# Performance work log

Measured on AMD Instinct MI355X. Metric: run time of the kernel, lower is better.

The kernel has to match this reference:

```python
import jax, jax.numpy as jnp
import numpy as np

THRESHOLD = 0.5
NEGPOS_RATIO = 3
VARIANCES = (0.1, 0.2)

B, P, C, T = 64, 24564, 81, 50


def point_form(boxes):
    # center form (cx,cy,w,h) -> corner form (x1,y1,x2,y2)
    return jnp.concatenate([boxes[:, :2] - boxes[:, 2:] / 2,
                            boxes[:, :2] + boxes[:, 2:] / 2], axis=-1)


def jaccard(box_a, box_b):
    # box_a [T,4], box_b [P,4], corner form -> IoU [T,P]
    max_xy = jnp.minimum(box_a[:, None, 2:], box_b[None, :, 2:])
    min_xy = jnp.maximum(box_a[:, None, :2], box_b[None, :, :2])
    inter = jnp.prod(jnp.clip(max_xy - min_xy, 0.0), axis=-1)
    area_a = jnp.prod(box_a[:, 2:] - box_a[:, :2], axis=-1)[:, None]
    area_b = jnp.prod(box_b[:, 2:] - box_b[:, :2], axis=-1)[None, :]
    return inter / (area_a + area_b - inter)


def encode(matched, priors, variances):
    # matched [P,4] corner form, priors [P,4] center form
    g_cxcy = (matched[:, :2] + matched[:, 2:]) / 2 - priors[:, :2]
    g_cxcy = g_cxcy / (variances[0] * priors[:, 2:])
    g_wh = (matched[:, 2:] - matched[:, :2]) / priors[:, 2:]
    g_wh = jnp.log(g_wh) / variances[1]
    return jnp.concatenate([g_cxcy, g_wh], axis=-1)


def match_one(truths, labels, priors):
    # truths [T,4] corner, labels [T] int, priors [P,4] center form
    overlaps = jaccard(truths, point_form(priors))          # [T,P]
    best_prior_idx = jnp.argmax(overlaps, axis=1)           # [T] best prior per gt
    best_truth_overlap = jnp.max(overlaps, axis=0)          # [P]
    best_truth_idx = jnp.argmax(overlaps, axis=0)           # [P]
    # ensure every gt keeps its best prior
    best_truth_overlap = best_truth_overlap.at[best_prior_idx].set(2.0)
    best_truth_idx = best_truth_idx.at[best_prior_idx].set(jnp.arange(truths.shape[0]))
    matched = truths[best_truth_idx]                        # [P,4]
    conf = labels[best_truth_idx] + 1                       # background = 0
    conf = jnp.where(best_truth_overlap < THRESHOLD, 0, conf)
    loc = encode(matched, priors, VARIANCES)                # [P,4]
    return loc, conf


def setup_inputs() -> dict:
    key = jax.random.key(0)
    k1, k2, k3, k4, k5, k6, k7 = jax.random.split(key, 7)
    loc_data = jax.random.normal(k1, (B, P, 4), jnp.float32)
    conf_data = jax.random.normal(k2, (B, P, C), jnp.float32)
    # priors: center form, in-bounds
    ctr = 0.05 + 0.9 * jax.random.uniform(k3, (P, 2))
    wh = 0.05 + 0.25 * jax.random.uniform(k4, (P, 2))
    priors = jnp.concatenate([ctr, wh], axis=-1).astype(jnp.float32)
    # gt boxes: corner form with x2>x1, y2>y1
    xy1 = 0.7 * jax.random.uniform(k5, (B, T, 2))
    gwh = 0.05 + 0.25 * jax.random.uniform(k6, (B, T, 2))
    targets_boxes = jnp.concatenate([xy1, jnp.minimum(xy1 + gwh, 1.0)], axis=-1).astype(jnp.float32)
    targets_labels = jax.random.randint(k7, (B, T), 0, C - 1, jnp.int32)
    return {"loc_data": loc_data, "conf_data": conf_data, "priors": priors,
            "targets_boxes": targets_boxes, "targets_labels": targets_labels}


def reference(loc_data, conf_data, priors, targets_boxes, targets_labels):
    num, num_priors, _ = loc_data.shape
    # per-image matching, batched with vmap
    loc_t, conf_t = jax.vmap(lambda t, l: match_one(t, l, priors))(targets_boxes, targets_labels)
    pos = conf_t > 0                                         # [B,P]
    # localization: smooth-L1 over positives, sum
    diff = loc_data - loc_t
    ad = jnp.abs(diff)
    sl1 = jnp.where(ad < 1.0, 0.5 * diff * diff, ad - 0.5)
    loss_l = jnp.sum(sl1 * pos[..., None])
    # confidence: cross entropy = logsumexp - gathered logit
    logsm = jax.nn.log_softmax(conf_data, axis=-1)
    ce = -jnp.take_along_axis(logsm, conf_t[..., None], axis=-1)[..., 0]  # [B,P]
    # hard negative mining: rank losses among negatives
    loss_mine = jnp.where(pos, 0.0, ce)
    num_pos = jnp.sum(pos, axis=1)                           # [B]
    num_neg = jnp.minimum(NEGPOS_RATIO * num_pos, num_priors - 1)
    idx_rank = jnp.argsort(jnp.argsort(-loss_mine, axis=1), axis=1)
    neg = idx_rank < num_neg[:, None]
    loss_c = jnp.sum(jnp.where(pos | neg, ce, 0.0))
    n = jnp.maximum(jnp.sum(num_pos), 1).astype(loc_data.dtype)
    return jnp.stack([loss_l / n, loss_c / n])
```

## Files before the change

### kernel.cpp

```cpp
#include <hip/hip_runtime.h>
#include <cstdint>
#include <cstddef>

#define NB 64
#define NP 24564
#define NC 81
#define NROWS (NB*NP)
#define NT 50
#define TCH 10
#define NSEG 16
#define SEGLEN 1536
#define RPB 128

__device__ __forceinline__ unsigned long long umax64(unsigned long long a, unsigned long long b){
  return a > b ? a : b;
}

__global__ __launch_bounds__(256) void k_bestprior(
    const float* __restrict__ priors, const float* __restrict__ tboxes,
    unsigned long long* __restrict__ bpk)
{
  __shared__ float tb[TCH*4];
  __shared__ float ta[TCH];
  __shared__ unsigned long long part[4][TCH];
  const int tid = threadIdx.x;
  const int b  = blockIdx.x;
  const int t0 = blockIdx.y * TCH;
  const int i0 = blockIdx.z * SEGLEN;
  const int iend = min(i0 + SEGLEN, NP);
  if (tid < TCH*4) tb[tid] = tboxes[(b*NT + t0)*4 + tid];
  __syncthreads();
  if (tid < TCH) ta[tid] = (tb[tid*4+2]-tb[tid*4+0]) * (tb[tid*4+3]-tb[tid*4+1]);
  __syncthreads();

  unsigned long long best[TCH];
  #pragma unroll
  for (int j = 0; j < TCH; ++j) best[j] = 0ULL;

  for (int i = i0 + tid; i < iend; i += 256){
    const float4 pr = ((const float4* __restrict__)priors)[i];
    const float px1 = pr.x - 0.5f*pr.z, py1 = pr.y - 0.5f*pr.w;
    const float px2 = pr.x + 0.5f*pr.z, py2 = pr.y + 0.5f*pr.w;
    const float pa  = pr.z * pr.w;
    const unsigned long long low = (unsigned long long)(~(unsigned)i);
    #pragma unroll
    for (int j = 0; j < TCH; ++j){
      float ix = fminf(tb[j*4+2], px2) - fmaxf(tb[j*4+0], px1);
      float iy = fminf(tb[j*4+3], py2) - fmaxf(tb[j*4+1], py1);
      ix = fmaxf(ix, 0.0f); iy = fmaxf(iy, 0.0f);
      const float inter = ix * iy;
      const float iou = inter / (ta[j] + pa - inter);
      const unsigned long long key =
          ((unsigned long long)__float_as_uint(iou) << 32) | low;
      best[j] = umax64(best[j], key);
    }
  }
  #pragma unroll
  for (int off = 32; off > 0; off >>= 1){
    #pragma unroll
    for (int j = 0; j < TCH; ++j)
      best[j] = umax64(best[j], __shfl_down(best[j], off));
  }
  const int wv = tid >> 6;
  if ((tid & 63) == 0){
    #pragma unroll
    for (int j = 0; j < TCH; ++j) part[wv][j] = best[j];
  }
  __syncthreads();
  if (tid < TCH){
    const unsigned long long m =
        umax64(umax64(part[0][tid], part[1][tid]),
               umax64(part[2][tid], part[3][tid]));
    atomicMax(&bpk[b*NT + t0 + tid], m);
  }
}

__global__ __launch_bounds__(256) void k_ce(
    const float* __restrict__ conf, const float* __restrict__ loc,
    const float* __restrict__ priors, const float* __restrict__ tboxes,
    const int* __restrict__ tlabels,
    const unsigned long long* __restrict__ bpk,
    float* __restrict__ mine, float* __restrict__ ce_pos,
    float* __restrict__ loss_l, int* __restrict__ num_pos)
{
  __shared__ float4 cbuf4[(RPB*NC)/4];
  __shared__ float tb[NT*4];
  __shared__ float ta[NT];
  __shared__ int ips[NT];
  __shared__ int tl[NT];
  float* cbuf = (float*)cbuf4;

  const int tid = threadIdx.x;
  const int b  = blockIdx.y;
  const int p0 = blockIdx.x * RPB;
  const int rows = min(RPB, NP - p0);

  if (tid < NT*4) tb[tid] = tboxes[b*NT*4 + tid];
  else if (tid < NT*4 + NT){
    const int t = tid - NT*4;
    ips[t] = (int)(~(unsigned)(bpk[b*NT + t] & 0xffffffffULL));
  }

  const float4* __restrict__ csrc =
      (const float4* __restrict__)(conf + (size_t)(b*NP + p0) * NC);
  const int nf4 = (rows * NC) >> 2;
  for (int i = tid; i < nf4; i += 256) cbuf4[i] = csrc[i];
  __syncthreads();
  if (tid < NT){
    ta[tid] = (tb[tid*4+2]-tb[tid*4+0]) * (tb[tid*4+3]-tb[tid*4+1]);
    tl[tid] = tlabels[b*NT + tid];
  }
  __syncthreads();

  const int row = tid >> 1;
  const int h   = tid & 1;
  const bool active = row < rows;
  const int p = p0 + (active ? row : 0);
  const int r = b*NP + p;

  const float4 pr = ((const float4* __restrict__)priors)[p];
  const float px1 = pr.x - 0.5f*pr.z, py1 = pr.y - 0.5f*pr.w;
  const float px2 = pr.x + 0.5f*pr.z, py2 = pr.y + 0.5f*pr.w;
  const float pa  = pr.z * pr.w;
  float ov = -1.0f; int ti = 0;
  for (int t = 0; t < NT; ++t){
    float ix = fminf(tb[t*4+2], px2) - fmaxf(tb[t*4+0], px1);
    float iy = fminf(tb[t*4+3], py2) - fmaxf(tb[t*4+1], py1);
    ix = fmaxf(ix, 0.0f); iy = fmaxf(iy, 0.0f);
    const float inter = ix * iy;
    const float iou = inter / (ta[t] + pa - inter);
    if (iou > ov){ ov = iou; ti = t; }
  }
  #pragma unroll 10
  for (int t = 0; t < NT; ++t){
    if (ips[t] == p){ ov = 2.0f; ti = t; }
  }
  const int cls = (ov < 0.5f) ? 0 : (tl[ti] + 1);

  const float* __restrict__ myrow = cbuf + row * NC;
  const int c0 = 41 * h;
  float v[41];
  #pragma unroll
  for (int c = 0; c < 40; ++c) v[c] = myrow[c0 + c];
  v[40] = h ? -INFINITY : myrow[40];

  float mh = v[0];
  #pragma unroll
  for (int c = 1; c < 41; ++c) mh = fmaxf(mh, v[c]);
  const float m = fmaxf(mh, __shfl_xor(mh, 1));

  float sh = 0.0f;
  #pragma unroll
  for (int c = 0; c < 41; ++c) sh += __expf(v[c] - m);
  const float S = sh + __shfl_xor(sh, 1);

  const float lg = myrow[cls];
  const float ce = m + __logf(S) - lg;

  const bool own = active && (h == 0);
  const bool pos = own && (cls > 0);
  if (own) mine[r] = pos ? 0.0f : ce;

  float cp = pos ? ce : 0.0f;
  float ll = 0.0f;
  int   pc = pos ? 1 : 0;
  if (pos){
    const float tx1 = tb[ti*4+0], ty1 = tb[ti*4+1], tx2 = tb[ti*4+2], ty2 = tb[ti*4+3];
    const float gcx = ((tx1 + tx2)*0.5f - pr.x) / (0.1f*pr.z);
    const float gcy = ((ty1 + ty2)*0.5f - pr.y) / (0.1f*pr.w);
    const float gw  = __logf((tx2 - tx1) / pr.z) * 5.0f;
    const float gh  = __logf((ty2 - ty1) / pr.w) * 5.0f;
    const float4 ld = ((const float4* __restrict__)loc)[r];
    float d, ad;
    d = ld.x - gcx; ad = fabsf(d); ll += (ad < 1.0f) ? 0.5f*d*d : ad - 0.5f;
    d = ld.y - gcy; ad = fabsf(d); ll += (ad < 1.0f) ? 0.5f*d*d : ad - 0.5f;
    d = ld.z - gw;  ad = fabsf(d); ll += (ad < 1.0f) ? 0.5f*d*d : ad - 0.5f;
    d = ld.w - gh;  ad = fabsf(d); ll += (ad < 1.0f) ? 0.5f*d*d : ad - 0.5f;
  }

  #pragma unroll
  for (int off = 32; off > 0; off >>= 1){
    cp += __shfl_down(cp, off);
    ll += __shfl_down(ll, off);
    pc += __shfl_down(pc, off);
  }
  __shared__ float rcp[4], rll[4];
  __shared__ int rpc[4];
  const int wv = tid >> 6;
  if ((tid & 63) == 0){ rcp[wv] = cp; rll[wv] = ll; rpc[wv] = pc; }
  __syncthreads();
  if (tid == 0){
    atomicAdd(&ce_pos[b], (rcp[0]+rcp[1])+(rcp[2]+rcp[3]));
    atomicAdd(&loss_l[b], (rll[0]+rll[1])+(rll[2]+rll[3]));
    atomicAdd(&num_pos[b], (rpc[0]+rpc[1])+(rpc[2]+rpc[3]));
  }
}

__global__ __launch_bounds__(1024) void k_topk(
    const float* __restrict__ mine, const int* __restrict__ num_pos,
    float* __restrict__ topk)
{
  const int b = blockIdx.x;
  const int tid = threadIdx.x;
  const float4* __restrict__ d4 =
      (const float4* __restrict__)(mine + (size_t)b * NP);
  const int k = min(3 * num_pos[b], NP - 1);

  __shared__ unsigned hist[256];
  __shared__ unsigned s_prefix;
  __shared__ int s_rem;
  __shared__ float wsum[16];

  if (k <= 0){
    if (tid == 0) topk[b] = 0.0f;
    return;
  }
  if (tid == 0){ s_prefix = 0u; s_rem = k; }

  for (int pass = 0; pass < 4; ++pass){
    const int shift = 24 - pass*8;
    if (tid < 256) hist[tid] = 0u;
    __syncthreads();
    const unsigned pref = s_prefix;
    const int rem = s_rem;
    for (int i = tid; i < 6141; i += 1024){
      const float4 v = d4[i];
      unsigned u;
      u = __float_as_uint(v.x);
      if (pass == 0 || (u >> (shift+8)) == pref) atomicAdd(&hist[(u>>shift)&255u], 1u);
      u = __float_as_uint(v.y);
      if (pass == 0 || (u >> (shift+8)) == pref) atomicAdd(&hist[(u>>shift)&255u], 1u);
      u = __float_as_uint(v.z);
      if (pass == 0 || (u >> (shift+8)) == pref) atomicAdd(&hist[(u>>shift)&255u], 1u);
      u = __float_as_uint(v.w);
      if (pass == 0 || (u >> (shift+8)) == pref) atomicAdd(&hist[(u>>shift)&255u], 1u);
    }
    __syncthreads();
    if (tid < 64){
      const unsigned h0 = hist[4*tid], h1 = hist[4*tid+1];
      const unsigned h2 = hist[4*tid+2], h3 = hist[4*tid+3];
      const unsigned pl = h0 + h1 + h2 + h3;
      unsigned S = pl;
      #pragma unroll
      for (int off = 1; off < 64; off <<= 1){
        const unsigned v = __shfl_down(S, off);
        if (tid + off < 64) S += v;
      }
      const unsigned Sn = S - pl;
      const unsigned t3 = h3 + Sn;
      const unsigned t2 = h2 + t3;
      const unsigned t1 = h1 + t2;
      const unsigned t0 = h0 + t1;
      if ((int)t0 >= rem && (int)t1 < rem){ s_prefix = (pref<<8) | (4u*tid+0u); s_rem = rem - (int)t1; }
      if ((int)t1 >= rem && (int)t2 < rem){ s_prefix = (pref<<8) | (4u*tid+1u); s_rem = rem - (int)t2; }
      if ((int)t2 >= rem && (int)t3 < rem){ s_prefix = (pref<<8) | (4u*tid+2u); s_rem = rem - (int)t3; }
      if ((int)t3 >= rem && (int)Sn < rem){ s_prefix = (pref<<8) | (4u*tid+3u); s_rem = rem - (int)Sn; }
    }
    __syncthreads();
  }

  const unsigned kb = s_prefix;
  const int rem = s_rem;
  const float kv = __uint_as_float(kb);
  float acc = 0.0f;
  for (int i = tid; i < 6141; i += 1024){
    const float4 v = d4[i];
    if (__float_as_uint(v.x) > kb) acc += v.x;
    if (__float_as_uint(v.y) > kb) acc += v.y;
    if (__float_as_uint(v.z) > kb) acc += v.z;
    if (__float_as_uint(v.w) > kb) acc += v.w;
  }
  #pragma unroll
  for (int off = 32; off > 0; off >>= 1) acc += __shfl_down(acc, off);
  if ((tid & 63) == 0) wsum[tid >> 6] = acc;
  __syncthreads();
  if (tid == 0){
    float s = 0.0f;
    #pragma unroll
    for (int j = 0; j < 16; ++j) s += wsum[j];
    topk[b] = s + (float)rem * kv;
  }
}

__global__ void k_final(const int* __restrict__ num_pos,
                        const float* __restrict__ loss_l,
                        const float* __restrict__ ce_pos,
                        const float* __restrict__ topk,
                        float* __restrict__ out)
{
  const int tid = threadIdx.x;
  int   np = num_pos[tid];
  float ll = loss_l[tid];
  float cp = ce_pos[tid];
  float tk = topk[tid];
  #pragma unroll
  for (int off = 32; off > 0; off >>= 1){
    np += __shfl_down(np, off);
    ll += __shfl_down(ll, off);
    cp += __shfl_down(cp, off);
    tk += __shfl_down(tk, off);
  }
  if (tid == 0){
    const float n = (float)max(np, 1);
    out[0] = ll / n;
    out[1] = (cp + tk) / n;
  }
}

extern "C" void kernel_launch(void* const* d_in, const int* in_sizes, int n_in,
                              void* d_out, int out_size, void* d_ws, size_t ws_size,
                              hipStream_t stream)
{
  const float* loc     = (const float*)d_in[0];
  const float* conf    = (const float*)d_in[1];
  const float* priors  = (const float*)d_in[2];
  const float* tboxes  = (const float*)d_in[3];
  const int*   tlabels = (const int*)d_in[4];
  float* out = (float*)d_out;

  char* ws = (char*)d_ws;
  int*   num_pos = (int*)(ws + 0);
  float* loss_l  = (float*)(ws + 256);
  float* ce_pos  = (float*)(ws + 512);
  float* topk    = (float*)(ws + 768);
  unsigned long long* bpk = (unsigned long long*)(ws + 1024);
  float* mine = (float*)(ws + 26624);

  hipMemsetAsync(ws, 0, 26624, stream);

  dim3 gA(NB, NT/TCH, NSEG);
  k_bestprior<<<gA, 256, 0, stream>>>(priors, tboxes, bpk);

  dim3 gC((NP + RPB - 1)/RPB, NB);
  k_ce<<<gC, 256, 0, stream>>>(conf, loc, priors, tboxes, tlabels,
                               bpk, mine, ce_pos, loss_l, num_pos);

  k_topk<<<NB, 1024, 0, stream>>>(mine, num_pos, topk);

  k_final<<<1, 64, 0, stream>>>(num_pos, loss_l, ce_pos, topk, out);
}
```

Measured before the change: 896.6 us.

## Halve rows per block, split each row across four lanes, prefetch conf into registers

The CE kernel now handles 64 rows per block with four lanes per row, each covering about 20 classes, so fewer registers are live per thread and shared memory per block is halved, which should let more blocks run per CU. The conf tile is loaded into registers first, then the target-box setup runs, then the registers are written to LDS, and one __syncthreads is removed. Target boxes are stored as float4. The cost is twice as many blocks, so per-block setup (IoU over 50 targets, each computed redundantly by all four lanes of a row) is repeated more often, plus an extra shuffle stage in the softmax reductions.

```diff
diff --git a/kernel.cpp b/kernel.cpp
--- a/kernel.cpp
+++ b/kernel.cpp
@@ -10,7 +10,7 @@
 #define TCH 10
 #define NSEG 16
 #define SEGLEN 1536
-#define RPB 128
+#define RPB 64
 
 __device__ __forceinline__ unsigned long long umax64(unsigned long long a, unsigned long long b){
   return a > b ? a : b;
@@ -83,8 +83,8 @@
     float* __restrict__ mine, float* __restrict__ ce_pos,
     float* __restrict__ loss_l, int* __restrict__ num_pos)
 {
-  __shared__ float4 cbuf4[(RPB*NC)/4];
-  __shared__ float tb[NT*4];
+  __shared__ float4 cbuf4[(RPB*NC)/4 + 1];
+  __shared__ float4 tb4[NT];
   __shared__ float ta[NT];
   __shared__ int ips[NT];
   __shared__ int tl[NT];
@@ -95,25 +95,35 @@
   const int p0 = blockIdx.x * RPB;
   const int rows = min(RPB, NP - p0);
 
-  if (tid < NT*4) tb[tid] = tboxes[b*NT*4 + tid];
-  else if (tid < NT*4 + NT){
-    const int t = tid - NT*4;
-    ips[t] = (int)(~(unsigned)(bpk[b*NT + t] & 0xffffffffULL));
-  }
-
   const float4* __restrict__ csrc =
       (const float4* __restrict__)(conf + (size_t)(b*NP + p0) * NC);
   const int nf4 = (rows * NC) >> 2;
-  for (int i = tid; i < nf4; i += 256) cbuf4[i] = csrc[i];
-  __syncthreads();
-  if (tid < NT){
-    ta[tid] = (tb[tid*4+2]-tb[tid*4+0]) * (tb[tid*4+3]-tb[tid*4+1]);
-    tl[tid] = tlabels[b*NT + tid];
-  }
-  __syncthreads();
-
-  const int row = tid >> 1;
-  const int h   = tid & 1;
+  float4 st[6];
+  #pragma unroll
+  for (int j = 0; j < 6; ++j){
+    const int i = tid + j*256;
+    if (i < nf4) st[j] = csrc[i];
+  }
+
+  if (tid < NT*4){
+    ((float*)tb4)[tid] = tboxes[b*NT*4 + tid];
+  } else if (tid < NT*4 + NT){
+    const int t = tid - NT*4;
+    const float4 T = ((const float4* __restrict__)tboxes)[b*NT + t];
+    ta[t] = (T.z - T.x) * (T.w - T.y);
+    tl[t] = tlabels[b*NT + t];
+    ips[t] = (int)(~(unsigned)(bpk[b*NT + t] & 0xffffffffULL));
+  }
+
+  #pragma unroll
+  for (int j = 0; j < 6; ++j){
+    const int i = tid + j*256;
+    if (i < nf4) cbuf4[i] = st[j];
+  }
+  __syncthreads();
+
+  const int row = tid >> 2;
+  const int q   = tid & 3;
   const bool active = row < rows;
   const int p = p0 + (active ? row : 0);
   const int r = b*NP + p;
@@ -124,8 +134,9 @@
   const float pa  = pr.z * pr.w;
   float ov = -1.0f; int ti = 0;
   for (int t = 0; t < NT; ++t){
-    float ix = fminf(tb[t*4+2], px2) - fmaxf(tb[t*4+0], px1);
-    float iy = fminf(tb[t*4+3], py2) - fmaxf(tb[t*4+1], py1);
+    const float4 T = tb4[t];
+    float ix = fminf(T.z, px2) - fmaxf(T.x, px1);
+    float iy = fminf(T.w, py2) - fmaxf(T.y, py1);
     ix = fmaxf(ix, 0.0f); iy = fmaxf(iy, 0.0f);
     const float inter = ix * iy;
     const float iou = inter / (ta[t] + pa - inter);
@@ -138,26 +149,29 @@
   const int cls = (ov < 0.5f) ? 0 : (tl[ti] + 1);
 
   const float* __restrict__ myrow = cbuf + row * NC;
-  const int c0 = 41 * h;
-  float v[41];
-  #pragma unroll
-  for (int c = 0; c < 40; ++c) v[c] = myrow[c0 + c];
-  v[40] = h ? -INFINITY : myrow[40];
+  const int c0 = q ? (1 + 20*q) : 0;
+  const int cnt = q ? 20 : 21;
+  float v[21];
+  #pragma unroll
+  for (int c = 0; c < 21; ++c)
+    v[c] = (c < cnt) ? myrow[c0 + c] : -INFINITY;
 
   float mh = v[0];
   #pragma unroll
-  for (int c = 1; c < 41; ++c) mh = fmaxf(mh, v[c]);
-  const float m = fmaxf(mh, __shfl_xor(mh, 1));
+  for (int c = 1; c < 21; ++c) mh = fmaxf(mh, v[c]);
+  float m = fmaxf(mh, __shfl_xor(mh, 1));
+  m = fmaxf(m, __shfl_xor(m, 2));
 
   float sh = 0.0f;
   #pragma unroll
-  for (int c = 0; c < 41; ++c) sh += __expf(v[c] - m);
-  const float S = sh + __shfl_xor(sh, 1);
+  for (int c = 0; c < 21; ++c) sh += __expf(v[c] - m);
+  float S = sh + __shfl_xor(sh, 1);
+  S += __shfl_xor(S, 2);
 
   const float lg = myrow[cls];
   const float ce = m + __logf(S) - lg;
 
-  const bool own = active && (h == 0);
+  const bool own = active && (q == 0);
   const bool pos = own && (cls > 0);
   if (own) mine[r] = pos ? 0.0f : ce;
 
@@ -165,11 +179,11 @@
   float ll = 0.0f;
   int   pc = pos ? 1 : 0;
   if (pos){
-    const float tx1 = tb[ti*4+0], ty1 = tb[ti*4+1], tx2 = tb[ti*4+2], ty2 = tb[ti*4+3];
-    const float gcx = ((tx1 + tx2)*0.5f - pr.x) / (0.1f*pr.z);
-    const float gcy = ((ty1 + ty2)*0.5f - pr.y) / (0.1f*pr.w);
-    const float gw  = __logf((tx2 - tx1) / pr.z) * 5.0f;
-    const float gh  = __logf((ty2 - ty1) / pr.w) * 5.0f;
+    const float4 T = tb4[ti];
+    const float gcx = ((T.x + T.z)*0.5f - pr.x) / (0.1f*pr.z);
+    const float gcy = ((T.y + T.w)*0.5f - pr.y) / (0.1f*pr.w);
+    const float gw  = __logf((T.z - T.x) / pr.z) * 5.0f;
+    const float gh  = __logf((T.w - T.y) / pr.w) * 5.0f;
     const float4 ld = ((const float4* __restrict__)loc)[r];
     float d, ad;
     d = ld.x - gcx; ad = fabsf(d); ll += (ad < 1.0f) ? 0.5f*d*d : ad - 0.5f;
```

After: 1.002 ms. +11.8%, slower.
